# Optimization experiments

Measured on AMD Instinct MI355X. Metric: run time of the kernel, lower is better.

The kernel has to match this reference:

```python
import math
import jax, jax.numpy as jnp
import numpy as np

L = 5  # local_context_length
H = 8  # heads


def _local_pool(x, L):
    """Causal local-window softmax pooling.
    For each position i, window = positions [i-L+1, i] (zero-padded at front),
    weights = softmax(x_i . x_window / sqrt(D)), pooled_i = sum_j w_ij * x_window_j.
    x: [B, S, D] -> [B, S, D]."""
    B, S, D = x.shape
    xp = jnp.pad(x, ((0, 0), (L - 1, 0), (0, 0)))          # [B, S+L-1, D]
    idx = jnp.arange(S)[:, None] + jnp.arange(L)[None, :]   # [S, L] window gather indices
    win = xp[:, idx, :]                                     # [B, S, L, D]
    scores = jnp.einsum('bsd,bsld->bsl', x, win) / jnp.asarray(math.sqrt(D), x.dtype)
    w = jax.nn.softmax(scores, axis=-1)                     # [B, S, L]
    return jnp.einsum('bsl,bsld->bsd', w, win)              # [B, S, D]


def setup_inputs() -> dict:
    key0 = jax.random.key(0)
    ks = jax.random.split(key0, 10)
    B, S, D = 4, 2048, 512
    scale = 1.0 / math.sqrt(D)
    return {
        'query': jax.random.normal(ks[0], (B, S, D), jnp.float32),
        'key':   jax.random.normal(ks[1], (B, S, D), jnp.float32),
        'value': jax.random.normal(ks[2], (B, S, D), jnp.float32),
        'mask':  jnp.ones((S, S), jnp.int32),  # dead: forward passes mask=None to attention
        'W_fk':  jax.random.normal(ks[3], (D, D), jnp.float32) * scale,
        'b_fk':  jnp.zeros((D,), jnp.float32),
        'W0':    jax.random.normal(ks[4], (D, D), jnp.float32) * scale,
        'b0':    jnp.zeros((D,), jnp.float32),
        'Wout':  jax.random.normal(ks[5], (D, D), jnp.float32) * scale,
        'bout':  jnp.zeros((D,), jnp.float32),
    }


def reference(query, key, value, mask, W_fk, b_fk, W0, b0, Wout, bout):
    B, S, D = query.shape
    dk = D // H

    q = _local_pool(query, L)                                # [B,S,D]
    k = _local_pool(key @ W_fk + b_fk, L)                    # feature_weight_linear then pool
    v = value @ W0 + b0                                      # linears[0]

    def split(x):  # [B,S,D] -> [B,H,S,dk]
        return x.reshape(B, S, H, dk).transpose(0, 2, 1, 3)

    qh, kh, vh = split(q), split(k), split(v)
    scores = jnp.einsum('bhqd,bhkd->bhqk', qh, kh) / jnp.asarray(math.sqrt(dk), q.dtype)
    p = jax.nn.softmax(scores, axis=-1)                      # mask=None, dropout off (eval)
    x = jnp.einsum('bhqk,bhkd->bhqd', p, vh)
    x = x.transpose(0, 2, 1, 3).reshape(B, S, D)
    return x @ Wout + bout                                   # linears[-1]
```

## Files before the change

### kernel.cpp

```cpp
#include <hip/hip_runtime.h>
#include <hip/hip_bf16.h>
#include <math.h>

#define B_  4
#define S_  2048
#define D_  512
#define H_  8
#define DK_ 64
#define BS_ (B_*S_)

using bf16x8 = __attribute__((ext_vector_type(8))) short;
using f32x4  = __attribute__((ext_vector_type(4))) float;
using f32x16 = __attribute__((ext_vector_type(16))) float;

typedef const __attribute__((address_space(1))) unsigned int gu32;
typedef __attribute__((address_space(3))) unsigned int lu32;

static __device__ inline unsigned short f2bf(float a) {
  union { __hip_bfloat16 h; unsigned short u; } x;
  x.h = __float2bfloat16(a); return x.u;
}
static __device__ inline float bf16f(unsigned short u) {
  union { unsigned u32; float f; } x; x.u32 = (unsigned)u << 16; return x.f;
}
static __device__ inline unsigned pk2(float a, float b) {
  unsigned r;
  asm("v_cvt_pk_bf16_f32 %0, %1, %2" : "=v"(r) : "v"(a), "v"(b));
  return r;
}
static __device__ inline float ex2(float a) {
  return __builtin_amdgcn_exp2f(a);
}

template <int SPLIT, int BF16OUT>
__global__ __launch_bounds__(256) void gemm_mfma_kernel(
    const float* __restrict__ A, const float* __restrict__ W,
    const float* __restrict__ bias, void* __restrict__ Cv) {
  const int bn = blockIdx.x;
  const int bm = blockIdx.y;
  const int tid = threadIdx.x;
  const int wv = tid >> 6, lane = tid & 63;
  const int c = lane & 15, g = lane >> 4;

  __shared__ unsigned short As[SPLIT + 1][128][72];
  __shared__ unsigned short Wt[SPLIT + 1][64][72];

  f32x4 acc[2][4];
#pragma unroll
  for (int rt = 0; rt < 2; ++rt)
#pragma unroll
    for (int ds = 0; ds < 4; ++ds) acc[rt][ds] = f32x4{0.f, 0.f, 0.f, 0.f};

  const int arow = tid >> 1, ah = (tid & 1) * 32;
  const int wn = tid & 63, wkg = (tid >> 6) * 16;

  for (int k0 = 0; k0 < D_; k0 += 64) {
    float af[32];
    const float* ag = A + ((size_t)(bm * 128 + arow)) * D_ + k0 + ah;
#pragma unroll
    for (int i = 0; i < 8; ++i) *(float4*)&af[i * 4] = *(const float4*)(ag + i * 4);
    float wf[16];
    const float* wg = W + (size_t)(k0 + wkg) * D_ + bn * 64 + wn;
#pragma unroll
    for (int i = 0; i < 16; ++i) wf[i] = wg[(size_t)i * D_];

    __syncthreads();
#pragma unroll
    for (int grp = 0; grp < 4; ++grp) {
      unsigned h[4], l[4];
#pragma unroll
      for (int p = 0; p < 4; ++p) {
        float f0 = af[grp * 8 + p * 2], f1 = af[grp * 8 + p * 2 + 1];
        h[p] = pk2(f0, f1);
        if constexpr (SPLIT)
          l[p] = pk2(f0 - bf16f((unsigned short)(h[p] & 0xffff)),
                     f1 - bf16f((unsigned short)(h[p] >> 16)));
      }
      uint4 uh; uh.x = h[0]; uh.y = h[1]; uh.z = h[2]; uh.w = h[3];
      *(uint4*)&As[0][arow][ah + grp * 8] = uh;
      if constexpr (SPLIT) {
        uint4 ul; ul.x = l[0]; ul.y = l[1]; ul.z = l[2]; ul.w = l[3];
        *(uint4*)&As[1][arow][ah + grp * 8] = ul;
      }
    }
#pragma unroll
    for (int grp = 0; grp < 2; ++grp) {
      unsigned h[4], l[4];
#pragma unroll
      for (int p = 0; p < 4; ++p) {
        float f0 = wf[grp * 8 + p * 2], f1 = wf[grp * 8 + p * 2 + 1];
        h[p] = pk2(f0, f1);
        if constexpr (SPLIT)
          l[p] = pk2(f0 - bf16f((unsigned short)(h[p] & 0xffff)),
                     f1 - bf16f((unsigned short)(h[p] >> 16)));
      }
      uint4 uh; uh.x = h[0]; uh.y = h[1]; uh.z = h[2]; uh.w = h[3];
      *(uint4*)&Wt[0][wn][wkg + grp * 8] = uh;
      if constexpr (SPLIT) {
        uint4 ul; ul.x = l[0]; ul.y = l[1]; ul.z = l[2]; ul.w = l[3];
        *(uint4*)&Wt[1][wn][wkg + grp * 8] = ul;
      }
    }
    __syncthreads();

#pragma unroll
    for (int ksub = 0; ksub < 2; ++ksub) {
      bf16x8 bh[2], bl[2];
#pragma unroll
      for (int rt = 0; rt < 2; ++rt) {
        bh[rt] = *(const bf16x8*)&As[0][wv * 32 + rt * 16 + c][ksub * 32 + g * 8];
        if constexpr (SPLIT)
          bl[rt] = *(const bf16x8*)&As[1][wv * 32 + rt * 16 + c][ksub * 32 + g * 8];
      }
#pragma unroll
      for (int ds = 0; ds < 4; ++ds) {
        bf16x8 ah_ = *(const bf16x8*)&Wt[0][ds * 16 + c][ksub * 32 + g * 8];
#pragma unroll
        for (int rt = 0; rt < 2; ++rt)
          acc[rt][ds] = __builtin_amdgcn_mfma_f32_16x16x32_bf16(ah_, bh[rt], acc[rt][ds], 0, 0, 0);
        if constexpr (SPLIT) {
          bf16x8 al_ = *(const bf16x8*)&Wt[1][ds * 16 + c][ksub * 32 + g * 8];
#pragma unroll
          for (int rt = 0; rt < 2; ++rt) {
            acc[rt][ds] = __builtin_amdgcn_mfma_f32_16x16x32_bf16(ah_, bl[rt], acc[rt][ds], 0, 0, 0);
            acc[rt][ds] = __builtin_amdgcn_mfma_f32_16x16x32_bf16(al_, bh[rt], acc[rt][ds], 0, 0, 0);
          }
        }
      }
    }
  }

#pragma unroll
  for (int rt = 0; rt < 2; ++rt) {
    const size_t m = (size_t)bm * 128 + wv * 32 + rt * 16 + c;
#pragma unroll
    for (int ds = 0; ds < 4; ++ds) {
      const int n = bn * 64 + ds * 16 + 4 * g;
      float4 bv = *(const float4*)&bias[n];
      float o0 = acc[rt][ds][0] + bv.x, o1 = acc[rt][ds][1] + bv.y;
      float o2 = acc[rt][ds][2] + bv.z, o3 = acc[rt][ds][3] + bv.w;
      if constexpr (BF16OUT) {
        uint2 p; p.x = pk2(o0, o1); p.y = pk2(o2, o3);
        *(uint2*)((unsigned short*)Cv + m * D_ + n) = p;
      } else {
        float4 o; o.x = o0; o.y = o1; o.z = o2; o.w = o3;
        *(float4*)((float*)Cv + m * D_ + n) = o;
      }
    }
  }
}

__global__ __launch_bounds__(256) void local_pool_kernel(
    const float* __restrict__ x, unsigned short* __restrict__ out,
    float oscale) {
  const int gtid = blockIdx.x * 256 + threadIdx.x;
  const int wave = gtid >> 6;
  const int lane = gtid & 63;
  if (wave >= BS_) return;
  const int b = wave / S_, s = wave % S_;
  const float* xrow = x + ((size_t)b * S_ + s) * D_;
  const int d0 = lane * 8;
  float xi[8];
  *(float4*)&xi[0] = *(const float4*)&xrow[d0];
  *(float4*)&xi[4] = *(const float4*)&xrow[d0 + 4];
  float win[5][8];
  float sc[5];
#pragma unroll
  for (int j = 0; j < 5; ++j) {
    int src = s - 4 + j;
    float part = 0.f;
    if (src >= 0) {
      const float* wr = x + ((size_t)b * S_ + src) * D_;
      *(float4*)&win[j][0] = *(const float4*)&wr[d0];
      *(float4*)&win[j][4] = *(const float4*)&wr[d0 + 4];
#pragma unroll
      for (int t = 0; t < 8; ++t) part += xi[t] * win[j][t];
    } else {
#pragma unroll
      for (int t = 0; t < 8; ++t) win[j][t] = 0.f;
    }
    sc[j] = part;
  }
#pragma unroll
  for (int off = 1; off < 64; off <<= 1) {
#pragma unroll
    for (int j = 0; j < 5; ++j) sc[j] += __shfl_xor(sc[j], off, 64);
  }
  const float scale = 0.04419417382415922f;
  float m = sc[0] * scale;
#pragma unroll
  for (int j = 1; j < 5; ++j) m = fmaxf(m, sc[j] * scale);
  float w[5], lsum = 0.f;
#pragma unroll
  for (int j = 0; j < 5; ++j) { w[j] = expf(sc[j] * scale - m); lsum += w[j]; }
  const float inv = oscale / lsum;
  float o[8] = {};
#pragma unroll
  for (int j = 0; j < 5; ++j)
#pragma unroll
    for (int t = 0; t < 8; ++t) o[t] += w[j] * win[j][t];
  unsigned short* orow = out + ((size_t)b * S_ + s) * D_;
  uint4 pk;
  pk.x = pk2(o[0] * inv, o[1] * inv);
  pk.y = pk2(o[2] * inv, o[3] * inv);
  pk.z = pk2(o[4] * inv, o[5] * inv);
  pk.w = pk2(o[6] * inv, o[7] * inv);
  *(uint4*)&orow[d0] = pk;
}

__global__ __launch_bounds__(256, 3) void attn_mfma32_kernel(
    const unsigned short* __restrict__ q, const unsigned short* __restrict__ k,
    const unsigned short* __restrict__ v, float* __restrict__ x) {
  const int bid = (blockIdx.x & 7) * 128 + (blockIdx.x >> 3);
  const int qb = bid & 31;
  const int h  = (bid >> 5) & 7;
  const int b  = bid >> 8;
  const int tid = threadIdx.x;
  const int w = tid >> 6, l = tid & 63;
  const int ql = l & 31, hi = l >> 5;
  const int wq = w & 1, wh = w >> 1;

  __shared__ __align__(16) unsigned short TileMem[4][64 * 64];
  char* KsB = (char*)TileMem[wh];
  char* VtB = (char*)TileMem[2 + wh];

  bf16x8 Qf[4];
  {
    const unsigned short* qg =
        q + ((size_t)b * S_ + qb * 64 + wq * 32 + ql) * D_ + h * 64 + hi * 8;
#pragma unroll
    for (int f = 0; f < 4; ++f) Qf[f] = *(const bf16x8*)(qg + f * 16);
  }

  f32x16 accO[2] = {};
  float m = -INFINITY, lsum = 0.f;

  const int lr8 = l >> 3, lc = l & 7;
  const unsigned short* kgl =
      k + ((size_t)b * S_ + wh * 1024 + wq * 32 + lr8) * D_ + h * 64 + ((lc ^ lr8) << 3);
  char* ldsK = (char*)TileMem[wh] + wq * 4096;

  const int sh = tid >> 7, st = tid & 127;
  const int vd = st & 63, vg2 = (st >> 6) & 1;
  const unsigned short* vg0 =
      v + ((size_t)b * S_ + sh * 1024 + vg2 * 32) * D_ + h * 64 + vd;
  char* VtS = (char*)TileMem[2 + sh];
  const int vb0 = vd * 128 + vg2 * 64, vmask = (vd & 7) << 4;

  unsigned rvp[16];
#pragma unroll
  for (int i = 0; i < 16; ++i) {
    unsigned lo = vg0[(size_t)(2 * i) * D_];
    unsigned hs = vg0[(size_t)(2 * i + 1) * D_];
    rvp[i] = lo | (hs << 16);
  }

  for (int kt = 0; kt < 16; ++kt) {
    __syncthreads();
    {
      const unsigned short* kp = kgl + (size_t)kt * 64 * D_;
#pragma unroll
      for (int j = 0; j < 4; ++j)
        __builtin_amdgcn_global_load_lds((gu32*)(kp + (size_t)j * 8 * D_),
                                         (lu32*)(ldsK + j * 1024), 16, 0, 0);
    }
#pragma unroll
    for (int i = 0; i < 4; ++i) {
      uint4 t_;
      t_.x = rvp[4 * i]; t_.y = rvp[4 * i + 1];
      t_.z = rvp[4 * i + 2]; t_.w = rvp[4 * i + 3];
      *(uint4*)(VtS + ((vb0 + i * 16) ^ vmask)) = t_;
    }
    __syncthreads();
    if (kt + 1 < 16) {
      const size_t koff = (size_t)(kt + 1) * 64 * D_;
#pragma unroll
      for (int i = 0; i < 16; ++i) {
        unsigned lo = vg0[koff + (size_t)(2 * i) * D_];
        unsigned hs = vg0[koff + (size_t)(2 * i + 1) * D_];
        rvp[i] = lo | (hs << 16);
      }
    }

    f32x16 sA = {}, sB = {};
    __builtin_amdgcn_s_setprio(1);
#pragma unroll
    for (int f = 0; f < 4; ++f) {
      bf16x8 a0 = *(const bf16x8*)(KsB + ((ql * 128 + f * 32 + hi * 16) ^ ((ql & 7) << 4)));
      bf16x8 a1 = *(const bf16x8*)(KsB + (((ql + 32) * 128 + f * 32 + hi * 16) ^ ((ql & 7) << 4)));
      sA = __builtin_amdgcn_mfma_f32_32x32x16_bf16(a0, Qf[f], sA, 0, 0, 0);
      sB = __builtin_amdgcn_mfma_f32_32x32x16_bf16(a1, Qf[f], sB, 0, 0, 0);
    }
    __builtin_amdgcn_s_setprio(0);

    float mx[8];
#pragma unroll
    for (int r = 0; r < 8; ++r)
      mx[r] = fmaxf(fmaxf(sA[r], sA[r + 8]), fmaxf(sB[r], sB[r + 8]));
    mx[0] = fmaxf(mx[0], mx[4]); mx[1] = fmaxf(mx[1], mx[5]);
    mx[2] = fmaxf(mx[2], mx[6]); mx[3] = fmaxf(mx[3], mx[7]);
    mx[0] = fmaxf(fmaxf(mx[0], mx[1]), fmaxf(mx[2], mx[3]));
    const float mt = fmaxf(mx[0], __shfl_xor(mx[0], 32, 64));
    if (!__all(mt <= m + 10.0f)) {
      const float mn = fmaxf(m, mt);
      const float corr = ex2(m - mn);
      m = mn;
      lsum *= corr;
#pragma unroll
      for (int dt = 0; dt < 2; ++dt)
#pragma unroll
        for (int r = 0; r < 16; ++r) accO[dt][r] *= corr;
    }

    unsigned WA[8], WB[8];
    float s0 = 0.f, s1 = 0.f, s2 = 0.f, s3 = 0.f;
#pragma unroll
    for (int t = 0; t < 4; ++t) {
      float a0 = ex2(sA[4 * t + 0] - m), a1 = ex2(sA[4 * t + 1] - m);
      float a2 = ex2(sA[4 * t + 2] - m), a3 = ex2(sA[4 * t + 3] - m);
      WA[2 * t] = pk2(a0, a1); WA[2 * t + 1] = pk2(a2, a3);
      s0 += a0 + a1; s1 += a2 + a3;
      float b0 = ex2(sB[4 * t + 0] - m), b1 = ex2(sB[4 * t + 1] - m);
      float b2 = ex2(sB[4 * t + 2] - m), b3 = ex2(sB[4 * t + 3] - m);
      WB[2 * t] = pk2(b0, b1); WB[2 * t + 1] = pk2(b2, b3);
      s2 += b0 + b1; s3 += b2 + b3;
    }
    lsum += (s0 + s1) + (s2 + s3);

#pragma unroll
    for (int kc = 0; kc < 4; ++kc) {
      unsigned w0 = (kc < 2) ? WA[(kc & 1) * 4 + 0] : WB[(kc & 1) * 4 + 0];
      unsigned w1 = (kc < 2) ? WA[(kc & 1) * 4 + 1] : WB[(kc & 1) * 4 + 1];
      unsigned w2 = (kc < 2) ? WA[(kc & 1) * 4 + 2] : WB[(kc & 1) * 4 + 2];
      unsigned w3 = (kc < 2) ? WA[(kc & 1) * 4 + 3] : WB[(kc & 1) * 4 + 3];
      asm volatile("v_permlane32_swap_b32 %0, %1" : "+v"(w0), "+v"(w2));
      asm volatile("v_permlane32_swap_b32 %0, %1" : "+v"(w1), "+v"(w3));
      union { unsigned u[4]; bf16x8 v8; } pb;
      pb.u[0] = w0; pb.u[1] = w1; pb.u[2] = w2; pb.u[3] = w3;
      __builtin_amdgcn_s_setprio(1);
#pragma unroll
      for (int dt = 0; dt < 2; ++dt) {
        const int vrow = dt * 32 + ql;
        bf16x8 va = *(const bf16x8*)(VtB + ((vrow * 128 + kc * 32 + hi * 16) ^ ((ql & 7) << 4)));
        accO[dt] = __builtin_amdgcn_mfma_f32_32x32x16_bf16(va, pb.v8, accO[dt], 0, 0, 0);
      }
      __builtin_amdgcn_s_setprio(0);
    }
  }

  float lw = lsum + __shfl_xor(lsum, 32, 64);
  __syncthreads();
  float* cb = (float*)TileMem + (size_t)wq * 2176 + (size_t)l * 34;
  if (wh == 1) {
#pragma unroll
    for (int dt = 0; dt < 2; ++dt)
#pragma unroll
      for (int r = 0; r < 16; ++r) cb[dt * 16 + r] = accO[dt][r];
    cb[32] = m; cb[33] = lw;
  }
  __syncthreads();
  if (wh == 0) {
    const float m1 = cb[32], l1 = cb[33];
    const float mn = fmaxf(m, m1);
    const float a0 = ex2(m - mn), a1 = ex2(m1 - mn);
    const float inv = 1.f / (lw * a0 + l1 * a1);
    float* xrow = x + ((size_t)b * S_ + qb * 64 + wq * 32 + ql) * D_ + h * 64;
#pragma unroll
    for (int dt = 0; dt < 2; ++dt)
#pragma unroll
      for (int g0 = 0; g0 < 4; ++g0) {
        float4 o;
        o.x = (accO[dt][4 * g0 + 0] * a0 + cb[dt * 16 + 4 * g0 + 0] * a1) * inv;
        o.y = (accO[dt][4 * g0 + 1] * a0 + cb[dt * 16 + 4 * g0 + 1] * a1) * inv;
        o.z = (accO[dt][4 * g0 + 2] * a0 + cb[dt * 16 + 4 * g0 + 2] * a1) * inv;
        o.w = (accO[dt][4 * g0 + 3] * a0 + cb[dt * 16 + 4 * g0 + 3] * a1) * inv;
        *(float4*)&xrow[dt * 32 + hi * 4 + g0 * 8] = o;
      }
  }
}

extern "C" void kernel_launch(void* const* d_in, const int* in_sizes, int n_in,
                              void* d_out, int out_size, void* d_ws, size_t ws_size,
                              hipStream_t stream) {
  const float* query = (const float*)d_in[0];
  const float* key   = (const float*)d_in[1];
  const float* value = (const float*)d_in[2];
  const float* W_fk = (const float*)d_in[4];
  const float* b_fk = (const float*)d_in[5];
  const float* W0   = (const float*)d_in[6];
  const float* b0   = (const float*)d_in[7];
  const float* Wout = (const float*)d_in[8];
  const float* bout = (const float*)d_in[9];
  float* out = (float*)d_out;

  char* ws = (char*)d_ws;
  float* kfk_f32   = (float*)ws;
  float* x_f32     = (float*)(ws + (16u << 20));
  unsigned short* k_bf16 = (unsigned short*)(ws + (32u << 20));
  unsigned short* v_bf16 = (unsigned short*)(ws + (40u << 20));
  unsigned short* q_bf16 = (unsigned short*)ws;

  dim3 mgrid(D_ / 64, BS_ / 128);
  dim3 pgrid(BS_ * 64 / 256);
  const float qscale = 0.125f * 1.4426950408889634f;

  gemm_mfma_kernel<1, 0><<<mgrid, 256, 0, stream>>>(key, W_fk, b_fk, kfk_f32);
  local_pool_kernel<<<pgrid, 256, 0, stream>>>(kfk_f32, k_bf16, 1.0f);
  gemm_mfma_kernel<0, 1><<<mgrid, 256, 0, stream>>>(value, W0, b0, v_bf16);
  local_pool_kernel<<<pgrid, 256, 0, stream>>>(query, q_bf16, qscale);
  attn_mfma32_kernel<<<dim3(B_ * H_ * (S_ / 64)), 256, 0, stream>>>(q_bf16, k_bf16, v_bf16, x_f32);
  gemm_mfma_kernel<1, 0><<<mgrid, 256, 0, stream>>>(x_f32, Wout, bout, out);
}
```

Baseline: 183.9 us.

## Write V transposed from GEMM and double-buffer K/V tiles via async LDS loads

The V projection GEMM now writes its bf16 output transposed ([B, D, S]). The attention kernel can then fetch V tiles with direct global-to-LDS loads, like K, instead of gathering 16-bit elements through registers and transposing them into shared memory. The attention kernel double-buffers K and V in LDS and issues the next tile's loads before computing on the current one, with one barrier per iteration. In exchange the GEMM epilogue does scattered 2-byte strided stores, LDS use doubles, and the occupancy hint drops from 3 to 2 blocks.

```diff
diff --git a/kernel.cpp b/kernel.cpp
--- a/kernel.cpp
+++ b/kernel.cpp
@@ -32,7 +32,7 @@
   return __builtin_amdgcn_exp2f(a);
 }
 
-template <int SPLIT, int BF16OUT>
+template <int SPLIT, int OUTMODE>
 __global__ __launch_bounds__(256) void gemm_mfma_kernel(
     const float* __restrict__ A, const float* __restrict__ W,
     const float* __restrict__ bias, void* __restrict__ Cv) {
@@ -139,9 +139,17 @@
       float4 bv = *(const float4*)&bias[n];
       float o0 = acc[rt][ds][0] + bv.x, o1 = acc[rt][ds][1] + bv.y;
       float o2 = acc[rt][ds][2] + bv.z, o3 = acc[rt][ds][3] + bv.w;
-      if constexpr (BF16OUT) {
+      if constexpr (OUTMODE == 1) {
         uint2 p; p.x = pk2(o0, o1); p.y = pk2(o2, o3);
         *(uint2*)((unsigned short*)Cv + m * D_ + n) = p;
+      } else if constexpr (OUTMODE == 2) {
+        const unsigned u01 = pk2(o0, o1), u23 = pk2(o2, o3);
+        unsigned short* base =
+            (unsigned short*)Cv + ((size_t)(m >> 11) * D_ + n) * (size_t)S_ + (m & 2047);
+        base[0]        = (unsigned short)u01;
+        base[S_]       = (unsigned short)(u01 >> 16);
+        base[2 * S_]   = (unsigned short)u23;
+        base[3 * S_]   = (unsigned short)(u23 >> 16);
       } else {
         float4 o; o.x = o0; o.y = o1; o.z = o2; o.w = o3;
         *(float4*)((float*)Cv + m * D_ + n) = o;
@@ -208,9 +216,9 @@
   *(uint4*)&orow[d0] = pk;
 }
 
-__global__ __launch_bounds__(256, 3) void attn_mfma32_kernel(
+__global__ __launch_bounds__(256, 2) void attn_mfma32_kernel(
     const unsigned short* __restrict__ q, const unsigned short* __restrict__ k,
-    const unsigned short* __restrict__ v, float* __restrict__ x) {
+    const unsigned short* __restrict__ vt, float* __restrict__ x) {
   const int bid = (blockIdx.x & 7) * 128 + (blockIdx.x >> 3);
   const int qb = bid & 31;
   const int h  = (bid >> 5) & 7;
@@ -220,9 +228,7 @@
   const int ql = l & 31, hi = l >> 5;
   const int wq = w & 1, wh = w >> 1;
 
-  __shared__ __align__(16) unsigned short TileMem[4][64 * 64];
-  char* KsB = (char*)TileMem[wh];
-  char* VtB = (char*)TileMem[2 + wh];
+  __shared__ __align__(16) unsigned short L[2][2][2][4096];
 
   bf16x8 Qf[4];
   {
@@ -236,51 +242,36 @@
   float m = -INFINITY, lsum = 0.f;
 
   const int lr8 = l >> 3, lc = l & 7;
-  const unsigned short* kgl =
+  const unsigned short* kg =
       k + ((size_t)b * S_ + wh * 1024 + wq * 32 + lr8) * D_ + h * 64 + ((lc ^ lr8) << 3);
-  char* ldsK = (char*)TileMem[wh] + wq * 4096;
-
-  const int sh = tid >> 7, st = tid & 127;
-  const int vd = st & 63, vg2 = (st >> 6) & 1;
-  const unsigned short* vg0 =
-      v + ((size_t)b * S_ + sh * 1024 + vg2 * 32) * D_ + h * 64 + vd;
-  char* VtS = (char*)TileMem[2 + sh];
-  const int vb0 = vd * 128 + vg2 * 64, vmask = (vd & 7) << 4;
-
-  unsigned rvp[16];
-#pragma unroll
-  for (int i = 0; i < 16; ++i) {
-    unsigned lo = vg0[(size_t)(2 * i) * D_];
-    unsigned hs = vg0[(size_t)(2 * i + 1) * D_];
-    rvp[i] = lo | (hs << 16);
-  }
-
+  const unsigned short* vg =
+      vt + ((size_t)b * D_ + h * 64 + wq * 32 + lr8) * (size_t)S_ + wh * 1024 + ((lc ^ lr8) << 3);
+
+  auto ISSUE = [&](int t, int bf) {
+    const unsigned short* kp = kg + (size_t)t * 64 * D_;
+    const unsigned short* vp = vg + t * 64;
+    char* dk = (char*)&L[bf][0][wh][0] + wq * 4096;
+    char* dv = (char*)&L[bf][1][wh][0] + wq * 4096;
+#pragma unroll
+    for (int j = 0; j < 4; ++j) {
+      __builtin_amdgcn_global_load_lds((gu32*)(kp + (size_t)j * 8 * D_),
+                                       (lu32*)(dk + j * 1024), 16, 0, 0);
+      __builtin_amdgcn_global_load_lds((gu32*)(vp + (size_t)j * 8 * S_),
+                                       (lu32*)(dv + j * 1024), 16, 0, 0);
+    }
+  };
+
+  ISSUE(0, 0);
+  asm volatile("s_waitcnt vmcnt(0)" ::: "memory");
+  __builtin_amdgcn_s_barrier();
+  __builtin_amdgcn_sched_barrier(0);
+
+  int cur = 0;
   for (int kt = 0; kt < 16; ++kt) {
-    __syncthreads();
-    {
-      const unsigned short* kp = kgl + (size_t)kt * 64 * D_;
-#pragma unroll
-      for (int j = 0; j < 4; ++j)
-        __builtin_amdgcn_global_load_lds((gu32*)(kp + (size_t)j * 8 * D_),
-                                         (lu32*)(ldsK + j * 1024), 16, 0, 0);
-    }
-#pragma unroll
-    for (int i = 0; i < 4; ++i) {
-      uint4 t_;
-      t_.x = rvp[4 * i]; t_.y = rvp[4 * i + 1];
-      t_.z = rvp[4 * i + 2]; t_.w = rvp[4 * i + 3];
-      *(uint4*)(VtS + ((vb0 + i * 16) ^ vmask)) = t_;
-    }
-    __syncthreads();
-    if (kt + 1 < 16) {
-      const size_t koff = (size_t)(kt + 1) * 64 * D_;
-#pragma unroll
-      for (int i = 0; i < 16; ++i) {
-        unsigned lo = vg0[koff + (size_t)(2 * i) * D_];
-        unsigned hs = vg0[koff + (size_t)(2 * i + 1) * D_];
-        rvp[i] = lo | (hs << 16);
-      }
-    }
+    if (kt + 1 < 16) ISSUE(kt + 1, cur ^ 1);
+    __builtin_amdgcn_sched_barrier(0);
+    const char* KsB = (const char*)&L[cur][0][wh][0];
+    const char* VtB = (const char*)&L[cur][1][wh][0];
 
     f32x16 sA = {}, sB = {};
     __builtin_amdgcn_s_setprio(1);
@@ -346,11 +337,16 @@
       }
       __builtin_amdgcn_s_setprio(0);
     }
+
+    asm volatile("s_waitcnt vmcnt(0)" ::: "memory");
+    __builtin_amdgcn_s_barrier();
+    __builtin_amdgcn_sched_barrier(0);
+    cur ^= 1;
   }
 
   float lw = lsum + __shfl_xor(lsum, 32, 64);
   __syncthreads();
-  float* cb = (float*)TileMem + (size_t)wq * 2176 + (size_t)l * 34;
+  float* cb = (float*)L + (size_t)wq * 2176 + (size_t)l * 34;
   if (wh == 1) {
 #pragma unroll
     for (int dt = 0; dt < 2; ++dt)
@@ -397,7 +393,7 @@
   float* kfk_f32   = (float*)ws;
   float* x_f32     = (float*)(ws + (16u << 20));
   unsigned short* k_bf16 = (unsigned short*)(ws + (32u << 20));
-  unsigned short* v_bf16 = (unsigned short*)(ws + (40u << 20));
+  unsigned short* vT_bf16 = (unsigned short*)(ws + (40u << 20));
   unsigned short* q_bf16 = (unsigned short*)ws;
 
   dim3 mgrid(D_ / 64, BS_ / 128);
@@ -406,8 +402,8 @@
 
   gemm_mfma_kernel<1, 0><<<mgrid, 256, 0, stream>>>(key, W_fk, b_fk, kfk_f32);
   local_pool_kernel<<<pgrid, 256, 0, stream>>>(kfk_f32, k_bf16, 1.0f);
-  gemm_mfma_kernel<0, 1><<<mgrid, 256, 0, stream>>>(value, W0, b0, v_bf16);
+  gemm_mfma_kernel<0, 2><<<mgrid, 256, 0, stream>>>(value, W0, b0, vT_bf16);
   local_pool_kernel<<<pgrid, 256, 0, stream>>>(query, q_bf16, qscale);
-  attn_mfma32_kernel<<<dim3(B_ * H_ * (S_ / 64)), 256, 0, stream>>>(q_bf16, k_bf16, v_bf16, x_f32);
+  attn_mfma32_kernel<<<dim3(B_ * H_ * (S_ / 64)), 256, 0, stream>>>(q_bf16, k_bf16, vT_bf16, x_f32);
   gemm_mfma_kernel<1, 0><<<mgrid, 256, 0, stream>>>(x_f32, Wout, bout, out);
 }
```

Result: faster. 171.5 us (-6.7%).
